# Optimization experiments

Hardware: AMD Instinct MI355X
Metric: run time of the kernel (lower is better)

The kernel has to match this reference:

```python
import jax, jax.numpy as jnp
import numpy as np

D_MODEL = 256; N_HEADS = 8; N_LEVELS = 4; N_POINTS = 4; D_FFN = 1024
SHAPES = [(128, 128), (64, 64), (32, 32), (16, 16)]  # (H, W) per level, strides 8/16/32/64 of 1024x1024 input
B = 8; LQ = 1024
S_TOT = sum(h * w for h, w in SHAPES)


def setup_inputs() -> dict:
    key = jax.random.key(0)
    ks = iter(jax.random.split(key, 48))
    d = D_MODEL

    def f(shape, s=0.02):
        return jax.random.normal(next(ks), shape, dtype=jnp.float32) * s

    return {
        'tgt': f((B, LQ, d), 1.0),
        'query_pos': f((B, LQ, d), 1.0),
        'reference_points': jax.random.uniform(next(ks), (B, LQ, N_LEVELS, 2), dtype=jnp.float32),
        'src': f((B, S_TOT, d), 1.0),
        'w_in': f((3 * d, d)), 'b_in': jnp.zeros((3 * d,), jnp.float32),
        'w_out': f((d, d)), 'b_out': jnp.zeros((d,), jnp.float32),
        'ln1_g': jnp.ones((d,), jnp.float32), 'ln1_b': jnp.zeros((d,), jnp.float32),
        'ln2_g': jnp.ones((d,), jnp.float32), 'ln2_b': jnp.zeros((d,), jnp.float32),
        'ln3_g': jnp.ones((d,), jnp.float32), 'ln3_b': jnp.zeros((d,), jnp.float32),
        'w_val': f((d, d)), 'b_val': jnp.zeros((d,), jnp.float32),
        'w_off': f((N_HEADS * N_LEVELS * N_POINTS * 2, d), 0.002),
        'b_off': f((N_HEADS * N_LEVELS * N_POINTS * 2,), 0.5),
        'w_attw': f((N_HEADS * N_LEVELS * N_POINTS, d)),
        'b_attw': jnp.zeros((N_HEADS * N_LEVELS * N_POINTS,), jnp.float32),
        'w_oc': f((d, d)), 'b_oc': jnp.zeros((d,), jnp.float32),
        'w1': f((D_FFN, d)), 'b1': jnp.zeros((D_FFN,), jnp.float32),
        'w2': f((d, D_FFN)), 'b2': jnp.zeros((d,), jnp.float32),
        'spatial_shapes': jnp.array(SHAPES, dtype=jnp.int32),
    }


def layer_norm(x, g, b):
    mu = x.mean(-1, keepdims=True)
    var = ((x - mu) ** 2).mean(-1, keepdims=True)
    return (x - mu) * jax.lax.rsqrt(var + 1e-5) * g + b


def mha(tgt, query_pos, w_in, b_in, w_out, b_out):
    d = D_MODEL; Dh = d // N_HEADS
    Bs, Lq, _ = tgt.shape
    qk = tgt + query_pos
    q = (qk @ w_in[:d].T + b_in[:d]).reshape(Bs, Lq, N_HEADS, Dh)
    k = (qk @ w_in[d:2 * d].T + b_in[d:2 * d]).reshape(Bs, Lq, N_HEADS, Dh)
    v = (tgt @ w_in[2 * d:].T + b_in[2 * d:]).reshape(Bs, Lq, N_HEADS, Dh)
    attn = jax.nn.softmax(jnp.einsum('bqhd,bkhd->bhqk', q, k) / np.sqrt(Dh).astype(np.float32), axis=-1)
    o = jnp.einsum('bhqk,bkhd->bqhd', attn, v).reshape(Bs, Lq, d)
    return o @ w_out.T + b_out


def ms_deform_attn(value, loc, attw):
    # value [B,S,H,Dh]; loc [B,Lq,H,L,P,2] in [0,1]; attw [B,Lq,H,L,P]
    Bs, _, Hh, Dh = value.shape
    Lq = loc.shape[1]

    def to_hfirst(x):  # [B,Lq,Hh,P] -> [B,Hh,Lq*P,1]
        return jnp.transpose(x, (0, 2, 1, 3)).reshape(Bs, Hh, Lq * N_POINTS, 1)

    acc = jnp.zeros((Bs, Hh, Lq * N_POINTS, Dh), value.dtype)
    start = 0
    for l, (H_, W_) in enumerate(SHAPES):
        v = jnp.transpose(value[:, start:start + H_ * W_], (0, 2, 1, 3))  # [B,Hh,HW,Dh]
        start += H_ * W_
        ll = loc[:, :, :, l]  # [B,Lq,Hh,P,2]
        x = ll[..., 0] * W_ - 0.5
        y = ll[..., 1] * H_ - 0.5
        x0 = jnp.floor(x); y0 = jnp.floor(y)
        tx = x - x0; ty = y - y0

        def gather(xi, yi):
            valid = ((xi >= 0) & (xi < W_) & (yi >= 0) & (yi < H_)).astype(value.dtype)
            fi = (jnp.clip(yi, 0, H_ - 1) * W_ + jnp.clip(xi, 0, W_ - 1)).astype(jnp.int32)
            g = jnp.take_along_axis(v, to_hfirst(fi.astype(jnp.float32)).astype(jnp.int32), axis=2)
            return g * to_hfirst(valid)

        samp = (gather(x0, y0) * to_hfirst((1 - tx) * (1 - ty))
                + gather(x0 + 1, y0) * to_hfirst(tx * (1 - ty))
                + gather(x0, y0 + 1) * to_hfirst((1 - tx) * ty)
                + gather(x0 + 1, y0 + 1) * to_hfirst(tx * ty))
        acc = acc + samp * to_hfirst(attw[:, :, :, l])
    out = acc.reshape(Bs, Hh, Lq, N_POINTS, Dh).sum(3)  # [B,Hh,Lq,Dh]
    return jnp.transpose(out, (0, 2, 1, 3)).reshape(Bs, Lq, Hh * Dh)


def reference(tgt, query_pos, reference_points, src, w_in, b_in, w_out, b_out,
              ln1_g, ln1_b, ln2_g, ln2_b, ln3_g, ln3_b,
              w_val, b_val, w_off, b_off, w_attw, b_attw, w_oc, b_oc,
              w1, b1, w2, b2, spatial_shapes):
    Bs, Lq, d = tgt.shape
    Dh = d // N_HEADS
    # --- self attention (q=k=tgt+pos, v=tgt), residual + norm2 ---
    t2 = mha(tgt, query_pos, w_in, b_in, w_out, b_out)
    tgt = layer_norm(tgt + t2, ln2_g, ln2_b)
    # --- MSDeformAttn cross attention, residual + norm1 ---
    query = tgt + query_pos
    value = (src @ w_val.T + b_val).reshape(Bs, -1, N_HEADS, Dh)
    off = (query @ w_off.T + b_off).reshape(Bs, Lq, N_HEADS, N_LEVELS, N_POINTS, 2)
    aw = jax.nn.softmax((query @ w_attw.T + b_attw).reshape(Bs, Lq, N_HEADS, N_LEVELS * N_POINTS), axis=-1)
    aw = aw.reshape(Bs, Lq, N_HEADS, N_LEVELS, N_POINTS)
    normalizer = jnp.array([[w, h] for h, w in SHAPES], dtype=tgt.dtype)  # (W,H) per level
    loc = reference_points[:, :, None, :, None, :] + off / normalizer[None, None, None, :, None, :]
    ca = ms_deform_attn(value, loc, aw) @ w_oc.T + b_oc
    tgt = layer_norm(tgt + ca, ln1_g, ln1_b)
    # --- FFN, residual + norm3 ---
    t2 = jax.nn.relu(tgt @ w1.T + b1) @ w2.T + b2
    tgt = layer_norm(tgt + t2, ln3_g, ln3_b)
    return tgt
```

## Files before the change

kernel.cpp:

```cpp
#include <hip/hip_runtime.h>

typedef unsigned short ushort_t;
typedef unsigned int uint_t;
typedef __attribute__((ext_vector_type(8))) short short8;
typedef __attribute__((ext_vector_type(4))) float floatx4;
typedef __attribute__((ext_vector_type(4))) unsigned short ushortx4;

__device__ __forceinline__ ushort_t f2bf(float f){
  uint_t u = __builtin_bit_cast(uint_t, f);
  u += 0x7FFFu + ((u >> 16) & 1u);
  return (ushort_t)(u >> 16);
}
__device__ __forceinline__ float bf2f(ushort_t u){
  uint_t x = ((uint_t)u) << 16;
  return __builtin_bit_cast(float, x);
}
__device__ __forceinline__ uint_t packbf2(float a, float b){
  return (uint_t)f2bf(a) | ((uint_t)f2bf(b) << 16);
}

__device__ __forceinline__ void gload16(const void* g, void* l){
  __builtin_amdgcn_global_load_lds(
      (const __attribute__((address_space(1))) void*)g,
      (__attribute__((address_space(3))) void*)l, 16, 0, 0);
}

__global__ __launch_bounds__(256) void convert_w_kernel(const float* __restrict__ w_in_v,
    const float* __restrict__ w_val, const float* __restrict__ w_out,
    const float* __restrict__ w_oc, const float* __restrict__ w1,
    const float* __restrict__ w2, ushort_t* __restrict__ dst){
  int j = (blockIdx.x*256 + threadIdx.x) * 4;
  if (j >= 786432) return;
  const float* src; int off;
  if      (j <  65536){ src = w_in_v; off = 0;      }
  else if (j < 131072){ src = w_val;  off = 65536;  }
  else if (j < 196608){ src = w_out;  off = 131072; }
  else if (j < 262144){ src = w_oc;   off = 196608; }
  else if (j < 524288){ src = w1;     off = 262144; }
  else                { src = w2;     off = 524288; }
  float4 v = *(const float4*)(src + (j - off));
  uint2 u; u.x = packbf2(v.x, v.y); u.y = packbf2(v.z, v.w);
  *(uint2*)(dst + j) = u;
}

__global__ __launch_bounds__(256) void pack_offattw_kernel(const float* __restrict__ w_off,
    const float* __restrict__ w_attw, const float* __restrict__ b_off,
    const float* __restrict__ b_attw, float* __restrict__ dst){
  int j = (blockIdx.x*256 + threadIdx.x) * 4;
  if (j >= 98688) return;
  const float* src; int off;
  if      (j < 65536){ src = w_off;  off = 0;     }
  else if (j < 98304){ src = w_attw; off = 65536; }
  else if (j < 98560){ src = b_off;  off = 98304; }
  else               { src = b_attw; off = 98560; }
  *(float4*)(dst + j) = *(const float4*)(src + (j - off));
}

__global__ __launch_bounds__(256) void addln_kernel(const float* __restrict__ X,
    const float* __restrict__ Y, const float* __restrict__ gw,
    const float* __restrict__ bw, float* __restrict__ Out){
  int wave = threadIdx.x >> 6, lane = threadIdx.x & 63;
  long row = (long)blockIdx.x * 4 + wave;
  long base = row * 256 + lane * 4;
  float4 x = *(const float4*)(X + base);
  float4 y = *(const float4*)(Y + base);
  float v0=x.x+y.x, v1=x.y+y.y, v2=x.z+y.z, v3=x.w+y.w;
  float s  = v0+v1+v2+v3;
  float sq = v0*v0+v1*v1+v2*v2+v3*v3;
  #pragma unroll
  for (int off=32; off>0; off>>=1){
    s  += __shfl_xor(s, off);
    sq += __shfl_xor(sq, off);
  }
  float mu  = s * (1.f/256.f);
  float var = sq * (1.f/256.f) - mu*mu;
  float rs  = rsqrtf(var + 1e-5f);
  float4 g4 = *(const float4*)(gw + lane*4);
  float4 b4 = *(const float4*)(bw + lane*4);
  float4 o;
  o.x = (v0-mu)*rs*g4.x + b4.x;
  o.y = (v1-mu)*rs*g4.y + b4.y;
  o.z = (v2-mu)*rs*g4.z + b4.z;
  o.w = (v3-mu)*rs*g4.w + b4.w;
  *(float4*)(Out + base) = o;
}

__device__ __forceinline__ void stage_store(ushort_t* ls, int r, int c4, float4 v){
  int byte = r*64 + ((((c4>>1) ^ ((r>>1)&3)) << 4) | ((c4&1) << 3));
  uint2 u; u.x = packbf2(v.x, v.y); u.y = packbf2(v.z, v.w);
  *(uint2*)((char*)ls + byte) = u;
}
__device__ __forceinline__ short8 frag_load(const ushort_t* ls, int r, int g){
  int byte = r*64 + ((g ^ ((r>>1)&3)) << 4);
  return *(const short8*)((const char*)ls + byte);
}

__device__ __forceinline__ short8 frag_load_f32(const float* ls, int r, int g){
  const char* base = (const char*)ls + r*128;
  int x = r & 7;
  float4 f0 = *(const float4*)(base + ((((2*g)  ^ x)) << 4));
  float4 f1 = *(const float4*)(base + ((((2*g+1)^ x)) << 4));
  uint4 u;
  u.x = packbf2(f0.x, f0.y); u.y = packbf2(f0.z, f0.w);
  u.z = packbf2(f1.x, f1.y); u.w = packbf2(f1.z, f1.w);
  return __builtin_bit_cast(short8, u);
}

template<bool RELU, bool OUT_BF16>
__global__ __launch_bounds__(256) void gemm_dma_kernel(const float* __restrict__ A,
    const ushort_t* __restrict__ Wbf, const float* __restrict__ bias,
    void* __restrict__ Cout, int M, int N, int K){
  __shared__ float    ldsA[2][4096];
  __shared__ ushort_t ldsB[2][4096];
  const int t = threadIdx.x;
  const int lane = t & 63, wave = t >> 6;
  const int wm = wave >> 1, wn = wave & 1;
  const long rowA0 = (long)blockIdx.x * 128;
  const long rowB0 = (long)blockIdx.y * 128;
  const int rr = lane & 15, g = lane >> 4;
  const int arow  = lane >> 3;
  const int aslot = (lane & 7) ^ (arow & 7);
  const float* Abase = A + (rowA0 + wave*32 + arow)*(long)K + aslot*4;
  const int brow  = lane >> 2;
  const int bslot = lane & 3;
  floatx4 acc[4][4] = {};
  const int nsteps = K >> 5;

  #define ISSUE(kk, buf) do { \
    _Pragma("unroll") \
    for (int c=0;c<4;++c) \
      gload16(Abase + (kk) + (long)(8*c)*K, &ldsA[buf][(wave*32 + 8*c)*32]); \
    _Pragma("unroll") \
    for (int c=0;c<2;++c){ \
      int r_ = wave*32 + c*16 + brow; \
      const ushort_t* bs_ = Wbf + (rowB0 + r_)*(long)K + (kk) + (bslot ^ ((r_>>1)&3))*8; \
      gload16(bs_, (char*)ldsB[buf] + (wave*32 + c*16)*64); \
    } \
  } while(0)

  ISSUE(0, 0);
  if (nsteps > 1) ISSUE(32, 1);

  for (int k = 0; k < nsteps; ++k){
    if (k < nsteps-1) asm volatile("s_waitcnt vmcnt(6)" ::: "memory");
    else              asm volatile("s_waitcnt vmcnt(0)" ::: "memory");
    __builtin_amdgcn_s_barrier();
    const float*    lA = ldsA[k & 1];
    const ushort_t* lB = ldsB[k & 1];
    short8 af[4], bfr[4];
    #pragma unroll
    for (int mi=0;mi<4;++mi) af[mi]  = frag_load_f32(lA, wm*64 + mi*16 + rr, g);
    #pragma unroll
    for (int ni=0;ni<4;++ni) bfr[ni] = frag_load(lB, wn*64 + ni*16 + rr, g);
    #pragma unroll
    for (int mi=0;mi<4;++mi)
      #pragma unroll
      for (int ni=0;ni<4;++ni)
        acc[mi][ni] = __builtin_amdgcn_mfma_f32_16x16x32_bf16(af[mi], bfr[ni], acc[mi][ni], 0, 0, 0);
    __builtin_amdgcn_s_barrier();
    if (k + 2 < nsteps) ISSUE((k+2)*32, k & 1);
  }
  #undef ISSUE

  const int cg = lane >> 4;
  #pragma unroll
  for (int ni=0;ni<4;++ni){
    long n = rowB0 + wn*64 + ni*16 + (lane & 15);
    float bv = bias[n];
    #pragma unroll
    for (int mi=0;mi<4;++mi){
      long m = rowA0 + wm*64 + mi*16 + cg*4;
      #pragma unroll
      for (int r2=0;r2<4;++r2){
        float v = acc[mi][ni][r2] + bv;
        if (RELU) v = fmaxf(v, 0.f);
        if (OUT_BF16) ((ushort_t*)Cout)[(m+r2)*N + n] = f2bf(v);
        else          ((float*)Cout)[(m+r2)*N + n] = v;
      }
    }
  }
}

template<bool RELU, bool OUT_BF16>
__global__ __launch_bounds__(512, 4) void gemm_dma2_kernel(const float* __restrict__ A,
    const ushort_t* __restrict__ Wbf, const float* __restrict__ bias,
    void* __restrict__ Cout, int M, int N, int K){
  __shared__ float    ldsA[2][4096];
  __shared__ ushort_t ldsB[2][8192];
  const int t = threadIdx.x;
  const int lane = t & 63, wave = t >> 6;
  const int wm = wave >> 2, wn = wave & 3;
  const long rowA0 = (long)blockIdx.x * 128;
  const long n0 = (long)blockIdx.y * 256;
  const int rr = lane & 15, g = lane >> 4;
  const int arow_in = lane >> 3;
  const int aslot   = (lane & 7) ^ (arow_in & 7);
  const int brow_in = lane >> 2;
  const int bslot   = lane & 3;
  floatx4 acc[4][4] = {};
  const int nsteps = K >> 5;

  #define ISSUE2(kk, buf) do { \
    _Pragma("unroll") \
    for (int c=0;c<2;++c){ \
      int ar_ = (wave*2 + c)*8 + arow_in; \
      gload16(A + (rowA0 + ar_)*(long)K + (kk) + aslot*4, \
              &ldsA[buf][(wave*2 + c)*8*32]); \
    } \
    _Pragma("unroll") \
    for (int c=0;c<2;++c){ \
      int br_ = (wave*2 + c)*16 + brow_in; \
      const ushort_t* bs_ = Wbf + (n0 + br_)*(long)K + (kk) + (bslot ^ ((br_>>1)&3))*8; \
      gload16(bs_, (char*)ldsB[buf] + (wave*2 + c)*16*64); \
    } \
  } while(0)

  ISSUE2(0, 0);
  if (nsteps > 1) ISSUE2(32, 1);

  for (int k = 0; k < nsteps; ++k){
    if (k < nsteps-1) asm volatile("s_waitcnt vmcnt(4)" ::: "memory");
    else              asm volatile("s_waitcnt vmcnt(0)" ::: "memory");
    __builtin_amdgcn_s_barrier();
    const float*    lA = ldsA[k & 1];
    const ushort_t* lB = ldsB[k & 1];
    short8 af[4], bfr[4];
    #pragma unroll
    for (int mi=0;mi<4;++mi) af[mi]  = frag_load_f32(lA, wm*64 + mi*16 + rr, g);
    #pragma unroll
    for (int ni=0;ni<4;++ni) bfr[ni] = frag_load(lB, wn*64 + ni*16 + rr, g);
    #pragma unroll
    for (int mi=0;mi<4;++mi)
      #pragma unroll
      for (int ni=0;ni<4;++ni)
        acc[mi][ni] = __builtin_amdgcn_mfma_f32_16x16x32_bf16(af[mi], bfr[ni], acc[mi][ni], 0, 0, 0);
    __builtin_amdgcn_s_barrier();
    if (k + 2 < nsteps) ISSUE2((k+2)*32, k & 1);
  }
  #undef ISSUE2

  const int cg = lane >> 4;
  #pragma unroll
  for (int ni=0;ni<4;++ni){
    long n = n0 + wn*64 + ni*16 + (lane & 15);
    float bv = bias[n];
    #pragma unroll
    for (int mi=0;mi<4;++mi){
      long m = rowA0 + wm*64 + mi*16 + cg*4;
      #pragma unroll
      for (int r2=0;r2<4;++r2){
        float v = acc[mi][ni][r2] + bv;
        if (RELU) v = fmaxf(v, 0.f);
        if (OUT_BF16) ((ushort_t*)Cout)[(m+r2)*N + n] = f2bf(v);
        else          ((float*)Cout)[(m+r2)*N + n] = v;
      }
    }
  }
}

template<bool RELU>
__global__ __launch_bounds__(256) void gemm_add2_kernel(const float* __restrict__ A,
    const float* __restrict__ A2, const float* __restrict__ W,
    const float* __restrict__ bias, void* __restrict__ Cout,
    int M, int N, int K){
  __shared__ ushort_t lsA[4096], lsB[4096];
  const int t = threadIdx.x;
  const int lane = t & 63, wave = t >> 6;
  const int wm = wave >> 1, wn = wave & 1;
  const long rowA0 = (long)blockIdx.x * 128;
  const long rowB0 = (long)blockIdx.y * 128;
  floatx4 acc[4][4] = {};
  const int rr = lane & 15, g = lane >> 4;
  const int rA = t >> 3, c4 = t & 7;
  const float* Ap = A + (rowA0 + rA)*(long)K + c4*4;
  const float* A2p = A2 + (rowA0 + rA)*(long)K + c4*4;
  const float* Wp = W + (rowB0 + rA)*(long)K + c4*4;

  for (int k0 = 0; k0 < K; k0 += 32){
    __syncthreads();
    #pragma unroll
    for (int j=0;j<4;++j){
      float4 v = *(const float4*)(Ap + k0 + (long)(32*j)*K);
      float4 y = *(const float4*)(A2p + k0 + (long)(32*j)*K);
      v.x+=y.x; v.y+=y.y; v.z+=y.z; v.w+=y.w;
      stage_store(lsA, rA + 32*j, c4, v);
      stage_store(lsB, rA + 32*j, c4, *(const float4*)(Wp + k0 + (long)(32*j)*K));
    }
    __syncthreads();
    short8 af[4], bfr[4];
    #pragma unroll
    for (int mi=0;mi<4;++mi) af[mi]  = frag_load(lsA, wm*64 + mi*16 + rr, g);
    #pragma unroll
    for (int ni=0;ni<4;++ni) bfr[ni] = frag_load(lsB, wn*64 + ni*16 + rr, g);
    #pragma unroll
    for (int mi=0;mi<4;++mi)
      #pragma unroll
      for (int ni=0;ni<4;++ni)
        acc[mi][ni] = __builtin_amdgcn_mfma_f32_16x16x32_bf16(af[mi], bfr[ni], acc[mi][ni], 0, 0, 0);
  }
  const int cg = lane >> 4;
  #pragma unroll
  for (int ni=0;ni<4;++ni){
    long n = rowB0 + wn*64 + ni*16 + (lane & 15);
    float bv = bias[n];
    #pragma unroll
    for (int mi=0;mi<4;++mi){
      long m = rowA0 + wm*64 + mi*16 + cg*4;
      #pragma unroll
      for (int r2=0;r2<4;++r2){
        float v = acc[mi][ni][r2] + bv;
        if (RELU) v = fmaxf(v, 0.f);
        ((float*)Cout)[(m+r2)*N + n] = v;
      }
    }
  }
}

__global__ __launch_bounds__(256) void attn_mfma_kernel(const float* __restrict__ QK,
    const float* __restrict__ V, float* __restrict__ O){
  __shared__ ushort_t lsQ[4096];
  __shared__ ushort_t lsK[1024];
  __shared__ ushort_t lsVT[1024];
  __shared__ ushort_t lsP[4096];
  const int bh = blockIdx.y, b = bh >> 3, h = bh & 7;
  const int qt0 = blockIdx.x * 128;
  const int t = threadIdx.x, lane = t & 63, w = t >> 6;
  const int rr = lane & 15, g = lane >> 4;
  const float csc = 0.25506332f;

  const float* qbase = QK + ((long)b*1024 + qt0)*512 + h*32;
  #pragma unroll
  for (int j=0;j<4;++j){
    int i = t + j*256; int r = i>>3, c4i = i&7;
    float4 v = *(const float4*)(qbase + (long)r*512 + c4i*4);
    stage_store(lsQ, r, c4i, v);
  }
  __syncthreads();
  short8 bq[2];
  bq[0] = frag_load(lsQ, w*32 + rr, g);
  bq[1] = frag_load(lsQ, w*32 + 16 + rr, g);

  floatx4 accO[2][2] = {};
  float rsum[2] = {0.f, 0.f};
  const float* kbase = QK + (long)b*1024*512 + 256 + h*32;
  const float* vbase = V  + (long)b*1024*256 + h*32;

  for (int kt = 0; kt < 1024; kt += 32){
    __syncthreads();
    {
      int r = t >> 3, c4i = t & 7;
      float4 v = *(const float4*)(kbase + (long)(kt + r)*512 + c4i*4);
      stage_store(lsK, r, c4i, v);
    }
    {
      int kk = t >> 3, d4 = t & 7;
      float4 vv = *(const float4*)(vbase + (long)(kt + kk)*256 + d4*4);
      float vals[4] = {vv.x, vv.y, vv.z, vv.w};
      #pragma unroll
      for (int j=0;j<4;++j){
        int d = d4*4 + j;
        int cb = kk*2;
        int byte = d*64 + ((((cb>>4) ^ ((d>>1)&3)) << 4) | (cb & 15));
        *(ushort_t*)((char*)lsVT + byte) = f2bf(vals[j]);
      }
    }
    __syncthreads();
    floatx4 accS[2][2] = {};
    short8 ak0 = frag_load(lsK, rr, g);
    short8 ak1 = frag_load(lsK, 16 + rr, g);
    accS[0][0] = __builtin_amdgcn_mfma_f32_16x16x32_bf16(ak0, bq[0], accS[0][0], 0,0,0);
    accS[0][1] = __builtin_amdgcn_mfma_f32_16x16x32_bf16(ak0, bq[1], accS[0][1], 0,0,0);
    accS[1][0] = __builtin_amdgcn_mfma_f32_16x16x32_bf16(ak1, bq[0], accS[1][0], 0,0,0);
    accS[1][1] = __builtin_amdgcn_mfma_f32_16x16x32_bf16(ak1, bq[1], accS[1][1], 0,0,0);
    #pragma unroll
    for (int mi=0;mi<2;++mi){
      #pragma unroll
      for (int ni=0;ni<2;++ni){
        float p0 = exp2f(accS[mi][ni][0]*csc);
        float p1 = exp2f(accS[mi][ni][1]*csc);
        float p2 = exp2f(accS[mi][ni][2]*csc);
        float p3 = exp2f(accS[mi][ni][3]*csc);
        rsum[ni] += (p0+p1)+(p2+p3);
        int q   = w*32 + ni*16 + rr;
        int k0b = (mi*16 + g*4)*2;
        int byte = q*64 + ((((k0b>>4) ^ ((q>>1)&3)) << 4) | (k0b & 15));
        uint2 u; u.x = packbf2(p0,p1); u.y = packbf2(p2,p3);
        *(uint2*)((char*)lsP + byte) = u;
      }
    }
    short8 av0 = frag_load(lsVT, rr, g);
    short8 av1 = frag_load(lsVT, 16 + rr, g);
    short8 bp0 = frag_load(lsP, w*32 + rr, g);
    short8 bp1 = frag_load(lsP, w*32 + 16 + rr, g);
    accO[0][0] = __builtin_amdgcn_mfma_f32_16x16x32_bf16(av0, bp0, accO[0][0], 0,0,0);
    accO[0][1] = __builtin_amdgcn_mfma_f32_16x16x32_bf16(av0, bp1, accO[0][1], 0,0,0);
    accO[1][0] = __builtin_amdgcn_mfma_f32_16x16x32_bf16(av1, bp0, accO[1][0], 0,0,0);
    accO[1][1] = __builtin_amdgcn_mfma_f32_16x16x32_bf16(av1, bp1, accO[1][1], 0,0,0);
  }
  #pragma unroll
  for (int ni=0;ni<2;++ni){
    rsum[ni] += __shfl_xor(rsum[ni], 16);
    rsum[ni] += __shfl_xor(rsum[ni], 32);
    float inv = 1.f / rsum[ni];
    int q = qt0 + w*32 + ni*16 + rr;
    float* op = O + ((long)b*1024 + q)*256 + h*32;
    #pragma unroll
    for (int mi=0;mi<2;++mi){
      #pragma unroll
      for (int r2=0;r2<4;++r2){
        int d = mi*16 + g*4 + r2;
        op[d] = accO[mi][ni][r2] * inv;
      }
    }
  }
}

__global__ __launch_bounds__(256) void deform_kernel(const ushort_t* __restrict__ val,
    const float* __restrict__ offaw, const float* __restrict__ refp,
    float* __restrict__ Out){
  __shared__ float s_cat[1536], s_ref[32];
  const int t = threadIdx.x;
  const long q0 = (long)blockIdx.x * 4;
  const float* srcOA = offaw + q0*384;
  *(float4*)(s_cat + t*4) = *(const float4*)(srcOA + t*4);
  if (t < 128) *(float4*)(s_cat + 1024 + t*4) = *(const float4*)(srcOA + 1024 + t*4);
  if (t < 32)  s_ref[t] = refp[q0*8 + t];
  __syncthreads();
  const int qi = t >> 6, tl = t & 63;
  const int h = tl >> 3, dq = (tl & 7) << 2;
  const int bq = (int)q0 + qi;
  const int b = bq >> 10;
  const float* offp = s_cat + qi*384 + h*32;
  const float* awp  = s_cat + qi*384 + 256 + h*16;
  const float* refq = s_ref + qi*8;
  float mx = -1e30f;
  #pragma unroll
  for (int i=0;i<16;++i) mx = fmaxf(mx, awp[i]);
  float p[16], sum = 0.f;
  #pragma unroll
  for (int i=0;i<16;++i){ p[i] = expf(awp[i]-mx); sum += p[i]; }
  float inv = 1.f/sum;
  const long vb = (long)b*21760*256 + h*32 + dq;
  const int Dim[4] = {128,64,32,16};
  const int St[4]  = {0,16384,20480,21504};
  float a0=0.f, a1=0.f, a2=0.f, a3=0.f;
  #pragma unroll
  for (int l=0;l<4;++l){
    const int Wl = Dim[l], Hl = Dim[l], st = St[l];
    float rx = refq[2*l], ry = refq[2*l+1];
    #pragma unroll
    for (int pp=0;pp<4;++pp){
      float x = rx*(float)Wl + offp[l*8+pp*2]   - 0.5f;
      float y = ry*(float)Hl + offp[l*8+pp*2+1] - 0.5f;
      float xf = floorf(x), yf = floorf(y);
      int x0 = (int)xf, y0 = (int)yf;
      float tx = x - xf, ty = y - yf;
      float s0=0.f,s1=0.f,s2=0.f,s3=0.f;
      #define CORNER(XI, YI, WGT) { \
        int xi_ = (XI), yi_ = (YI); \
        bool valid_ = (xi_ >= 0) & (xi_ < Wl) & (yi_ >= 0) & (yi_ < Hl); \
        int xc_ = min(max(xi_, 0), Wl-1), yc_ = min(max(yi_, 0), Hl-1); \
        ushortx4 u = *(const ushortx4*)(val + vb + (long)(st + yc_*Wl + xc_)*256); \
        float wq = valid_ ? (WGT) : 0.f; \
        s0 += wq*bf2f(u[0]); s1 += wq*bf2f(u[1]); \
        s2 += wq*bf2f(u[2]); s3 += wq*bf2f(u[3]); \
      }
      CORNER(x0,   y0,   (1.f-tx)*(1.f-ty));
      CORNER(x0+1, y0,   tx*(1.f-ty));
      CORNER(x0,   y0+1, (1.f-tx)*ty);
      CORNER(x0+1, y0+1, tx*ty);
      #undef CORNER
      float pw = p[l*4+pp];
      a0 += pw*s0; a1 += pw*s1; a2 += pw*s2; a3 += pw*s3;
    }
  }
  float4 o; o.x=a0*inv; o.y=a1*inv; o.z=a2*inv; o.w=a3*inv;
  *(float4*)(Out + (long)bq*256 + h*32 + dq) = o;
}

extern "C" void kernel_launch(void* const* d_in, const int* in_sizes, int n_in,
                              void* d_out, int out_size, void* d_ws, size_t ws_size,
                              hipStream_t stream){
  (void)in_sizes; (void)n_in; (void)out_size; (void)ws_size;
  const float* tgt   = (const float*)d_in[0];
  const float* qpos  = (const float*)d_in[1];
  const float* refp  = (const float*)d_in[2];
  const float* src   = (const float*)d_in[3];
  const float* w_in  = (const float*)d_in[4];
  const float* b_in  = (const float*)d_in[5];
  const float* w_out = (const float*)d_in[6];
  const float* b_out = (const float*)d_in[7];
  const float* ln1g  = (const float*)d_in[8];
  const float* ln1b  = (const float*)d_in[9];
  const float* ln2g  = (const float*)d_in[10];
  const float* ln2b  = (const float*)d_in[11];
  const float* ln3g  = (const float*)d_in[12];
  const float* ln3b  = (const float*)d_in[13];
  const float* w_val = (const float*)d_in[14];
  const float* b_val = (const float*)d_in[15];
  const float* w_off = (const float*)d_in[16];
  const float* b_off = (const float*)d_in[17];
  const float* w_attw= (const float*)d_in[18];
  const float* b_attw= (const float*)d_in[19];
  const float* w_oc  = (const float*)d_in[20];
  const float* b_oc  = (const float*)d_in[21];
  const float* w1    = (const float*)d_in[22];
  const float* b1    = (const float*)d_in[23];
  const float* w2    = (const float*)d_in[24];
  const float* b2    = (const float*)d_in[25];

  float* ws = (float*)d_ws;
  float* bufQK  = ws + 2097152;
  float* bufOA  = ws + 2097152;
  float* bufV   = ws + 6291456;
  float* bufO   = ws + 8388608;
  float* bufT2  = ws + 10485760;
  float* bufTg1 = ws + 12582912;
  float* bufTg2 = ws + 14680064;
  ushort_t* bufVal = (ushort_t*)(ws + 16777216);
  float* bufH   = ws + 16777216;
  ushort_t* bufWbf = (ushort_t*)(ws + 39059456);
  float* bufWOA = ws + 39452672;
  float* outF   = (float*)d_out;

  const ushort_t* winvbf = bufWbf;
  const ushort_t* wvalbf = bufWbf + 65536;
  const ushort_t* woutbf = bufWbf + 131072;
  const ushort_t* wocbf  = bufWbf + 196608;
  const ushort_t* w1bf   = bufWbf + 262144;
  const ushort_t* w2bf   = bufWbf + 524288;

  dim3 B256(256), B512(512);
  convert_w_kernel<<<dim3(768), B256, 0, stream>>>(w_in + 512*256, w_val, w_out, w_oc, w1, w2, bufWbf);
  pack_offattw_kernel<<<dim3(97), B256, 0, stream>>>(w_off, w_attw, b_off, b_attw, bufWOA);
  gemm_add2_kernel<false><<<dim3(64,4), B256, 0, stream>>>(tgt, qpos, w_in, b_in, bufQK, 8192, 512, 256);
  gemm_dma_kernel<false,false><<<dim3(64,2), B256, 0, stream>>>(tgt, winvbf, b_in + 512, bufV, 8192, 256, 256);
  attn_mfma_kernel<<<dim3(8,64), B256, 0, stream>>>(bufQK, bufV, bufO);
  gemm_dma_kernel<false,false><<<dim3(64,2), B256, 0, stream>>>(bufO, woutbf, b_out, bufT2, 8192, 256, 256);
  addln_kernel<<<dim3(2048), B256, 0, stream>>>(tgt, bufT2, ln2g, ln2b, bufTg1);
  gemm_dma2_kernel<false,true><<<dim3(1360,1), B512, 0, stream>>>(src, wvalbf, b_val, bufVal, 174080, 256, 256);
  gemm_add2_kernel<false><<<dim3(64,3), B256, 0, stream>>>(bufTg1, qpos, bufWOA, bufWOA + 98304, bufOA, 8192, 384, 256);
  deform_kernel<<<dim3(2048), B256, 0, stream>>>(bufVal, bufOA, refp, bufO);
  gemm_dma_kernel<false,false><<<dim3(64,2), B256, 0, stream>>>(bufO, wocbf, b_oc, bufT2, 8192, 256, 256);
  addln_kernel<<<dim3(2048), B256, 0, stream>>>(bufTg1, bufT2, ln1g, ln1b, bufTg2);
  gemm_dma2_kernel<true,false><<<dim3(64,4), B512, 0, stream>>>(bufTg2, w1bf, b1, bufH, 8192, 1024, 256);
  gemm_dma2_kernel<false,false><<<dim3(64,1), B512, 0, stream>>>(bufH, w2bf, b2, bufT2, 8192, 256, 1024);
  addln_kernel<<<dim3(2048), B256, 0, stream>>>(bufTg2, bufT2, ln3g, ln3b, outF);
}
```

Before: 317.6 us.

## Store QK/V projections in bf16 and use 64-row GEMM tiles for N=256 GEMMs

The Q/K and V projection GEMMs now write bf16 outputs, and the attention kernel loads bf16 directly. This halves the bytes it reads and removes the per-element conversion during staging. The N=256 GEMMs, including the FFN down projection, move to a new variant with 64-row tiles and twice as many blocks, which should fill more compute units. The LDS barriers become asm s_barrier with memory clobbers. Rounding QK/V to bf16 earlier slightly changes numerics, and smaller tiles reload the weight tile more often.

```diff
diff --git a/kernel.cpp b/kernel.cpp
--- a/kernel.cpp
+++ b/kernel.cpp
@@ -24,6 +24,8 @@
       (const __attribute__((address_space(1))) void*)g,
       (__attribute__((address_space(3))) void*)l, 16, 0, 0);
 }
+
+#define FENCED_BARRIER() asm volatile("s_barrier" ::: "memory")
 
 __global__ __launch_bounds__(256) void convert_w_kernel(const float* __restrict__ w_in_v,
     const float* __restrict__ w_val, const float* __restrict__ w_out,
@@ -90,6 +92,10 @@
   uint2 u; u.x = packbf2(v.x, v.y); u.y = packbf2(v.z, v.w);
   *(uint2*)((char*)ls + byte) = u;
 }
+__device__ __forceinline__ void stage_copy16(ushort_t* ls, int r, int s, short8 v){
+  int byte = r*64 + ((s ^ ((r>>1)&3)) << 4);
+  *(short8*)((char*)ls + byte) = v;
+}
 __device__ __forceinline__ short8 frag_load(const ushort_t* ls, int r, int g){
   int byte = r*64 + ((g ^ ((r>>1)&3)) << 4);
   return *(const short8*)((const char*)ls + byte);
@@ -107,60 +113,62 @@
 }
 
 template<bool RELU, bool OUT_BF16>
-__global__ __launch_bounds__(256) void gemm_dma_kernel(const float* __restrict__ A,
+__global__ __launch_bounds__(256) void gemm_dma3_kernel(const float* __restrict__ A,
     const ushort_t* __restrict__ Wbf, const float* __restrict__ bias,
     void* __restrict__ Cout, int M, int N, int K){
-  __shared__ float    ldsA[2][4096];
+  __shared__ float    ldsA[2][2048];
   __shared__ ushort_t ldsB[2][4096];
   const int t = threadIdx.x;
   const int lane = t & 63, wave = t >> 6;
   const int wm = wave >> 1, wn = wave & 1;
-  const long rowA0 = (long)blockIdx.x * 128;
+  const long rowA0 = (long)blockIdx.x * 64;
   const long rowB0 = (long)blockIdx.y * 128;
   const int rr = lane & 15, g = lane >> 4;
-  const int arow  = lane >> 3;
-  const int aslot = (lane & 7) ^ (arow & 7);
-  const float* Abase = A + (rowA0 + wave*32 + arow)*(long)K + aslot*4;
-  const int brow  = lane >> 2;
-  const int bslot = lane & 3;
-  floatx4 acc[4][4] = {};
+  const int arow_in = lane >> 3;
+  const int aslot   = (lane & 7) ^ (arow_in & 7);
+  const int brow_in = lane >> 2;
+  const int bslot   = lane & 3;
+  floatx4 acc[2][4] = {};
   const int nsteps = K >> 5;
 
-  #define ISSUE(kk, buf) do { \
-    _Pragma("unroll") \
-    for (int c=0;c<4;++c) \
-      gload16(Abase + (kk) + (long)(8*c)*K, &ldsA[buf][(wave*32 + 8*c)*32]); \
+  #define ISSUE3(kk, buf) do { \
     _Pragma("unroll") \
     for (int c=0;c<2;++c){ \
-      int r_ = wave*32 + c*16 + brow; \
-      const ushort_t* bs_ = Wbf + (rowB0 + r_)*(long)K + (kk) + (bslot ^ ((r_>>1)&3))*8; \
+      int ar_ = wave*16 + c*8 + arow_in; \
+      gload16(A + (rowA0 + ar_)*(long)K + (kk) + aslot*4, \
+              &ldsA[buf][(wave*16 + c*8)*32]); \
+    } \
+    _Pragma("unroll") \
+    for (int c=0;c<2;++c){ \
+      int br_ = wave*32 + c*16 + brow_in; \
+      const ushort_t* bs_ = Wbf + (rowB0 + br_)*(long)K + (kk) + (bslot ^ ((br_>>1)&3))*8; \
       gload16(bs_, (char*)ldsB[buf] + (wave*32 + c*16)*64); \
     } \
   } while(0)
 
-  ISSUE(0, 0);
-  if (nsteps > 1) ISSUE(32, 1);
+  ISSUE3(0, 0);
+  if (nsteps > 1) ISSUE3(32, 1);
 
   for (int k = 0; k < nsteps; ++k){
-    if (k < nsteps-1) asm volatile("s_waitcnt vmcnt(6)" ::: "memory");
+    if (k < nsteps-1) asm volatile("s_waitcnt vmcnt(4)" ::: "memory");
     else              asm volatile("s_waitcnt vmcnt(0)" ::: "memory");
-    __builtin_amdgcn_s_barrier();
+    FENCED_BARRIER();
     const float*    lA = ldsA[k & 1];
     const ushort_t* lB = ldsB[k & 1];
-    short8 af[4], bfr[4];
-    #pragma unroll
-    for (int mi=0;mi<4;++mi) af[mi]  = frag_load_f32(lA, wm*64 + mi*16 + rr, g);
+    short8 af[2], bfr[4];
+    #pragma unroll
+    for (int mi=0;mi<2;++mi) af[mi]  = frag_load_f32(lA, wm*32 + mi*16 + rr, g);
     #pragma unroll
     for (int ni=0;ni<4;++ni) bfr[ni] = frag_load(lB, wn*64 + ni*16 + rr, g);
     #pragma unroll
-    for (int mi=0;mi<4;++mi)
+    for (int mi=0;mi<2;++mi)
       #pragma unroll
       for (int ni=0;ni<4;++ni)
         acc[mi][ni] = __builtin_amdgcn_mfma_f32_16x16x32_bf16(af[mi], bfr[ni], acc[mi][ni], 0, 0, 0);
-    __builtin_amdgcn_s_barrier();
-    if (k + 2 < nsteps) ISSUE((k+2)*32, k & 1);
-  }
-  #undef ISSUE
+    FENCED_BARRIER();
+    if (k + 2 < nsteps) ISSUE3((k+2)*32, k & 1);
+  }
+  #undef ISSUE3
 
   const int cg = lane >> 4;
   #pragma unroll
@@ -168,8 +176,8 @@
     long n = rowB0 + wn*64 + ni*16 + (lane & 15);
     float bv = bias[n];
     #pragma unroll
-    for (int mi=0;mi<4;++mi){
-      long m = rowA0 + wm*64 + mi*16 + cg*4;
+    for (int mi=0;mi<2;++mi){
+      long m = rowA0 + wm*32 + mi*16 + cg*4;
       #pragma unroll
       for (int r2=0;r2<4;++r2){
         float v = acc[mi][ni][r2] + bv;
@@ -221,7 +229,7 @@
   for (int k = 0; k < nsteps; ++k){
     if (k < nsteps-1) asm volatile("s_waitcnt vmcnt(4)" ::: "memory");
     else              asm volatile("s_waitcnt vmcnt(0)" ::: "memory");
-    __builtin_amdgcn_s_barrier();
+    FENCED_BARRIER();
     const float*    lA = ldsA[k & 1];
     const ushort_t* lB = ldsB[k & 1];
     short8 af[4], bfr[4];
@@ -234,7 +242,7 @@
       #pragma unroll
       for (int ni=0;ni<4;++ni)
         acc[mi][ni] = __builtin_amdgcn_mfma_f32_16x16x32_bf16(af[mi], bfr[ni], acc[mi][ni], 0, 0, 0);
-    __builtin_amdgcn_s_barrier();
+    FENCED_BARRIER();
     if (k + 2 < nsteps) ISSUE2((k+2)*32, k & 1);
   }
   #undef ISSUE2
@@ -258,7 +266,7 @@
   }
 }
 
-template<bool RELU>
+template<bool RELU, bool OUT_BF16>
 __global__ __launch_bounds__(256) void gemm_add2_kernel(const float* __restrict__ A,
     const float* __restrict__ A2, const float* __restrict__ W,
     const float* __restrict__ bias, void* __restrict__ Cout,
@@ -310,14 +318,15 @@
       for (int r2=0;r2<4;++r2){
         float v = acc[mi][ni][r2] + bv;
         if (RELU) v = fmaxf(v, 0.f);
-        ((float*)Cout)[(m+r2)*N + n] = v;
-      }
-    }
-  }
-}
-
-__global__ __launch_bounds__(256) void attn_mfma_kernel(const float* __restrict__ QK,
-    const float* __restrict__ V, float* __restrict__ O){
+        if (OUT_BF16) ((ushort_t*)Cout)[(m+r2)*N + n] = f2bf(v);
+        else          ((float*)Cout)[(m+r2)*N + n] = v;
+      }
+    }
+  }
+}
+
+__global__ __launch_bounds__(256) void attn_mfma_kernel(const ushort_t* __restrict__ QK,
+    const ushort_t* __restrict__ V, float* __restrict__ O){
   __shared__ ushort_t lsQ[4096];
   __shared__ ushort_t lsK[1024];
   __shared__ ushort_t lsVT[1024];
@@ -328,12 +337,12 @@
   const int rr = lane & 15, g = lane >> 4;
   const float csc = 0.25506332f;
 
-  const float* qbase = QK + ((long)b*1024 + qt0)*512 + h*32;
-  #pragma unroll
-  for (int j=0;j<4;++j){
-    int i = t + j*256; int r = i>>3, c4i = i&7;
-    float4 v = *(const float4*)(qbase + (long)r*512 + c4i*4);
-    stage_store(lsQ, r, c4i, v);
+  const ushort_t* qbase = QK + ((long)b*1024 + qt0)*512 + h*32;
+  #pragma unroll
+  for (int j=0;j<2;++j){
+    int i = t + j*256; int r = i>>2, s = i&3;
+    short8 v = *(const short8*)(qbase + (long)r*512 + s*8);
+    stage_copy16(lsQ, r, s, v);
   }
   __syncthreads();
   short8 bq[2];
@@ -342,26 +351,25 @@
 
   floatx4 accO[2][2] = {};
   float rsum[2] = {0.f, 0.f};
-  const float* kbase = QK + (long)b*1024*512 + 256 + h*32;
-  const float* vbase = V  + (long)b*1024*256 + h*32;
+  const ushort_t* kbase = QK + (long)b*1024*512 + 256 + h*32;
+  const ushort_t* vbase = V  + (long)b*1024*256 + h*32;
 
   for (int kt = 0; kt < 1024; kt += 32){
     __syncthreads();
-    {
-      int r = t >> 3, c4i = t & 7;
-      float4 v = *(const float4*)(kbase + (long)(kt + r)*512 + c4i*4);
-      stage_store(lsK, r, c4i, v);
+    if (t < 128){
+      int r = t >> 2, s = t & 3;
+      short8 v = *(const short8*)(kbase + (long)(kt + r)*512 + s*8);
+      stage_copy16(lsK, r, s, v);
     }
     {
       int kk = t >> 3, d4 = t & 7;
-      float4 vv = *(const float4*)(vbase + (long)(kt + kk)*256 + d4*4);
-      float vals[4] = {vv.x, vv.y, vv.z, vv.w};
+      ushortx4 vv = *(const ushortx4*)(vbase + (long)(kt + kk)*256 + d4*4);
       #pragma unroll
       for (int j=0;j<4;++j){
         int d = d4*4 + j;
         int cb = kk*2;
         int byte = d*64 + ((((cb>>4) ^ ((d>>1)&3)) << 4) | (cb & 15));
-        *(ushort_t*)((char*)lsVT + byte) = f2bf(vals[j]);
+        *(ushort_t*)((char*)lsVT + byte) = vv[j];
       }
     }
     __syncthreads();
@@ -510,9 +518,9 @@
   const float* b2    = (const float*)d_in[25];
 
   float* ws = (float*)d_ws;
-  float* bufQK  = ws + 2097152;
+  ushort_t* bufQK = (ushort_t*)(ws + 2097152);
   float* bufOA  = ws + 2097152;
-  float* bufV   = ws + 6291456;
+  ushort_t* bufV = (ushort_t*)(ws + 6291456);
   float* bufO   = ws + 8388608;
   float* bufT2  = ws + 10485760;
   float* bufTg1 = ws + 12582912;
@@ -533,17 +541,17 @@
   dim3 B256(256), B512(512);
   convert_w_kernel<<<dim3(768), B256, 0, stream>>>(w_in + 512*256, w_val, w_out, w_oc, w1, w2, bufWbf);
   pack_offattw_kernel<<<dim3(97), B256, 0, stream>>>(w_off, w_attw, b_off, b_attw, bufWOA);
-  gemm_add2_kernel<false><<<dim3(64,4), B256, 0, stream>>>(tgt, qpos, w_in, b_in, bufQK, 8192, 512, 256);
-  gemm_dma_kernel<false,false><<<dim3(64,2), B256, 0, stream>>>(tgt, winvbf, b_in + 512, bufV, 8192, 256, 256);
+  gemm_add2_kernel<false,true><<<dim3(64,4), B256, 0, stream>>>(tgt, qpos, w_in, b_in, bufQK, 8192, 512, 256);
+  gemm_dma3_kernel<false,true><<<dim3(128,2), B256, 0, stream>>>(tgt, winvbf, b_in + 512, bufV, 8192, 256, 256);
   attn_mfma_kernel<<<dim3(8,64), B256, 0, stream>>>(bufQK, bufV, bufO);
-  gemm_dma_kernel<false,false><<<dim3(64,2), B256, 0, stream>>>(bufO, woutbf, b_out, bufT2, 8192, 256, 256);
+  gemm_dma3_kernel<false,false><<<dim3(128,2), B256, 0, stream>>>(bufO, woutbf, b_out, bufT2, 8192, 256, 256);
   addln_kernel<<<dim3(2048), B256, 0, stream>>>(tgt, bufT2, ln2g, ln2b, bufTg1);
   gemm_dma2_kernel<false,true><<<dim3(1360,1), B512, 0, stream>>>(src, wvalbf, b_val, bufVal, 174080, 256, 256);
-  gemm_add2_kernel<false><<<dim3(64,3), B256, 0, stream>>>(bufTg1, qpos, bufWOA, bufWOA + 98304, bufOA, 8192, 384, 256);
+  gemm_add2_kernel<false,false><<<dim3(64,3), B256, 0, stream>>>(bufTg1, qpos, bufWOA, bufWOA + 98304, bufOA, 8192, 384, 256);
   deform_kernel<<<dim3(2048), B256, 0, stream>>>(bufVal, bufOA, refp, bufO);
-  gemm_dma_kernel<false,false><<<dim3(64,2), B256, 0, stream>>>(bufO, wocbf, b_oc, bufT2, 8192, 256, 256);
+  gemm_dma3_kernel<false,false><<<dim3(128,2), B256, 0, stream>>>(bufO, wocbf, b_oc, bufT2, 8192, 256, 256);
   addln_kernel<<<dim3(2048), B256, 0, stream>>>(bufTg1, bufT2, ln1g, ln1b, bufTg2);
   gemm_dma2_kernel<true,false><<<dim3(64,4), B512, 0, stream>>>(bufTg2, w1bf, b1, bufH, 8192, 1024, 256);
-  gemm_dma2_kernel<false,false><<<dim3(64,1), B512, 0, stream>>>(bufH, w2bf, b2, bufT2, 8192, 256, 1024);
+  gemm_dma3_kernel<false,false><<<dim3(128,2), B256, 0, stream>>>(bufH, w2bf, b2, bufT2, 8192, 256, 1024);
   addln_kernel<<<dim3(2048), B256, 0, stream>>>(bufTg2, bufT2, ln3g, ln3b, outF);
 }
```

Result: faster. 290.9 us (-8.4%).
